# Optimization experiments

Measured on AMD Instinct MI355X. Metric: run time of the kernel, lower is better.

## Reference

```python
import jax, jax.numpy as jnp
import numpy as np

NUM_HEADS = 16
LN_EPS = 1e-5


def setup_inputs() -> dict:
    key = jax.random.key(0)
    ks = jax.random.split(key, 6)
    b, s, d = 2, 2048, 1024
    scale = 1.0 / np.sqrt(d)
    return {
        "x": jax.random.normal(ks[0], (b, s, d), dtype=jnp.float32),
        "W_w": jax.random.normal(ks[1], (3 * d, d), dtype=jnp.float32) * scale,
        "W_b": jax.random.normal(ks[2], (3 * d,), dtype=jnp.float32) * 0.01,
        "proj_w": jax.random.normal(ks[3], (d, d), dtype=jnp.float32) * scale,
        "proj_b": jax.random.normal(ks[4], (d,), dtype=jnp.float32) * 0.01,
        "gamma": jnp.ones((d,), dtype=jnp.float32),
        "beta": jnp.zeros((d,), dtype=jnp.float32),
    }


def reference(x, W_w, W_b, proj_w, proj_b, gamma, beta):
    b, s, d = x.shape
    h = NUM_HEADS
    hd = d // h
    # fused QKV projection: [b,s,3d]
    qkv = x @ W_w.T + W_b
    q, k, v = jnp.split(qkv, 3, axis=-1)
    # [b,s,d] -> [b,h,s,hd]
    q, k, v = (z.reshape(b, s, h, hd).transpose(0, 2, 1, 3) for z in (q, k, v))
    # NOTE: original scales by sqrt(d), not sqrt(head_dim)
    attn = jnp.einsum('bhqd,bhkd->bhqk', q, k) / jnp.sqrt(jnp.asarray(d, x.dtype))
    attn_weights = jax.nn.softmax(attn, axis=-1)  # [b,h,s,s]
    o = jnp.einsum('bhqk,bhkd->bhqd', attn_weights, v)
    o = o.transpose(0, 2, 1, 3).reshape(b, s, d)
    out = o @ proj_w.T + proj_b  # dropout is identity at eval
    y = x + out
    mu = jnp.mean(y, axis=-1, keepdims=True)
    var = jnp.var(y, axis=-1, keepdims=True)
    y_norm = (y - mu) / jnp.sqrt(var + LN_EPS) * gamma + beta
    return (y_norm, attn_weights)
```

## Files before the change

### kernel.cpp

```cpp
#include <hip/hip_runtime.h>
#include <cstdint>

#define BB 2
#define SS 2048
#define DD 1024
#define HH 16
#define HDIM 64
#define MM (BB*SS)
#define N3 (3*DD)

typedef __attribute__((ext_vector_type(4))) float f32x4;
typedef __attribute__((ext_vector_type(8))) __bf16 bf16x8;

static __device__ __forceinline__ unsigned short f2bf_fast(float f) {
  __bf16 h = (__bf16)f;
  return __builtin_bit_cast(unsigned short, h);
}

static __device__ __forceinline__ uint4 pack8f(const float4 a, const float4 b) {
  union { unsigned short us[8]; uint4 v; } pk;
  pk.us[0] = f2bf_fast(a.x); pk.us[1] = f2bf_fast(a.y); pk.us[2] = f2bf_fast(a.z); pk.us[3] = f2bf_fast(a.w);
  pk.us[4] = f2bf_fast(b.x); pk.us[5] = f2bf_fast(b.y); pk.us[6] = f2bf_fast(b.z); pk.us[7] = f2bf_fast(b.w);
  return pk.v;
}

static __device__ __forceinline__ void gload16(const unsigned short* g, unsigned short* l) {
  __builtin_amdgcn_global_load_lds(
      (const __attribute__((address_space(1))) void*)g,
      (__attribute__((address_space(3))) void*)l, 16, 0, 0);
}

__global__ __launch_bounds__(256) void cvt_kernel(
    const float* __restrict__ x, const float* __restrict__ Ww,
    const float* __restrict__ pw,
    unsigned short* __restrict__ xb, unsigned short* __restrict__ Wwb,
    unsigned short* __restrict__ pwb) {
  const size_t i = ((size_t)blockIdx.x * 256 + threadIdx.x) * 8;
  const float* src;
  unsigned short* dst;
  if (i < 4194304u)       { src = x  + i;            dst = xb  + i; }
  else if (i < 7340032u)  { src = Ww + (i - 4194304u); dst = Wwb + (i - 4194304u); }
  else                    { src = pw + (i - 7340032u); dst = pwb + (i - 7340032u); }
  const float4* s4 = (const float4*)src;
  *(uint4*)dst = pack8f(s4[0], s4[1]);
}

__global__ __launch_bounds__(256) void gemm_qkv(
    const unsigned short* __restrict__ xb, const unsigned short* __restrict__ Wwb,
    const float* __restrict__ Wb,
    unsigned short* __restrict__ qb, unsigned short* __restrict__ kb,
    unsigned short* __restrict__ vbT) {
  __shared__ __align__(16) unsigned short As[128 * 32];
  __shared__ __align__(16) unsigned short Bs[128 * 32];
  const int t = threadIdx.x;
  const int l = t & 63, w = t >> 6;
  const int wr = w >> 1, wc = w & 1;
  const int m0 = blockIdx.y * 128, n0 = blockIdx.x * 128;
  f32x4 acc[4][4] = {};

  for (int kt = 0; kt < DD; kt += 32) {
    __syncthreads();
    #pragma unroll
    for (int i = 0; i < 2; ++i) {
      const int row = (i * 4 + w) * 16 + (l >> 2);
      const int cc = (l & 3) * 8;
      gload16(xb  + (size_t)(m0 + row) * DD + kt + cc, &As[(i * 4 + w) * 512]);
      gload16(Wwb + (size_t)(n0 + row) * DD + kt + cc, &Bs[(i * 4 + w) * 512]);
    }
    __syncthreads();
    bf16x8 a[4], b[4];
    #pragma unroll
    for (int i = 0; i < 4; ++i) {
      a[i] = __builtin_bit_cast(bf16x8, *(const uint4*)&As[(wr * 64 + i * 16 + (l & 15)) * 32 + (l >> 4) * 8]);
      b[i] = __builtin_bit_cast(bf16x8, *(const uint4*)&Bs[(wc * 64 + i * 16 + (l & 15)) * 32 + (l >> 4) * 8]);
    }
    #pragma unroll
    for (int i = 0; i < 4; ++i)
      #pragma unroll
      for (int j = 0; j < 4; ++j)
        acc[i][j] = __builtin_amdgcn_mfma_f32_16x16x32_bf16(a[i], b[j], acc[i][j], 0, 0, 0);
  }

  #pragma unroll
  for (int i = 0; i < 4; ++i)
    #pragma unroll
    for (int j = 0; j < 4; ++j)
      #pragma unroll
      for (int r = 0; r < 4; ++r) {
        const int row = m0 + wr * 64 + i * 16 + (l >> 4) * 4 + r;
        const int col = n0 + wc * 64 + j * 16 + (l & 15);
        const float v = acc[i][j][r] + Wb[col];
        const int bidx = row >> 11;
        const int srow = row & 2047;
        const int which = col >> 10;
        const int cc = col & 1023;
        const int head = cc >> 6;
        const int hd = cc & 63;
        if (which == 0) {
          qb[((size_t)((bidx * HH + head) * SS + srow)) * HDIM + hd] = f2bf_fast(v * 0.03125f);
        } else if (which == 1) {
          kb[((size_t)((bidx * HH + head) * SS + srow)) * HDIM + hd] = f2bf_fast(v);
        } else {
          vbT[((size_t)(bidx * HH + head) * HDIM + hd) * SS + srow] = f2bf_fast(v);
        }
      }
}

__global__ __launch_bounds__(256) void attn_kernel(
    const unsigned short* __restrict__ qb,
    const unsigned short* __restrict__ kb,
    const unsigned short* __restrict__ vbT,
    unsigned short* __restrict__ ob,
    float* __restrict__ attn_out) {
  __shared__ __align__(16) unsigned short Ks[2][64 * 72];
  __shared__ __align__(16) unsigned short Vts[2][64 * 72];
  __shared__ __align__(16) unsigned short Ps[4 * 16 * 72];
  const int t = threadIdx.x;
  const int l = t & 63, w = t >> 6;
  const int bh = blockIdx.y;
  const int q0 = blockIdx.x * 64;
  const size_t base = (size_t)bh * SS * HDIM;

  bf16x8 qa[2];
  #pragma unroll
  for (int kc = 0; kc < 2; ++kc)
    qa[kc] = __builtin_bit_cast(bf16x8,
        *(const uint4*)(qb + base + (size_t)(q0 + w * 16 + (l & 15)) * HDIM + kc * 32 + (l >> 4) * 8));

  const int srow = t >> 2;
  const int scol = (t & 3) * 16;
  const unsigned short* kg = kb + base + (size_t)srow * HDIM + scol;
  const unsigned short* vg = vbT + ((size_t)bh * HDIM + srow) * SS + scol;

  float lsum[4] = {0.f, 0.f, 0.f, 0.f};

  {
    const uint4* g = (const uint4*)kg;
    uint4 a0 = g[0], a1 = g[1];
    uint4* d = (uint4*)&Ks[0][srow * 72 + scol];
    d[0] = a0; d[1] = a1;
  }
  __syncthreads();
  for (int kt = 0; kt < SS; kt += 64) {
    const int cur = (kt >> 6) & 1;
    const bool more = (kt + 64) < SS;
    uint4 a0, a1;
    if (more) {
      const uint4* g = (const uint4*)(kg + (size_t)(kt + 64) * HDIM);
      a0 = g[0]; a1 = g[1];
    }
    f32x4 sf[4] = {};
    __builtin_amdgcn_s_setprio(1);
    #pragma unroll
    for (int kc = 0; kc < 2; ++kc)
      #pragma unroll
      for (int n = 0; n < 4; ++n) {
        bf16x8 kf = __builtin_bit_cast(bf16x8, *(const uint4*)&Ks[cur][(n * 16 + (l & 15)) * 72 + kc * 32 + (l >> 4) * 8]);
        sf[n] = __builtin_amdgcn_mfma_f32_16x16x32_bf16(qa[kc], kf, sf[n], 0, 0, 0);
      }
    __builtin_amdgcn_s_setprio(0);
    #pragma unroll
    for (int r = 0; r < 4; ++r)
      lsum[r] += __expf(sf[0][r]) + __expf(sf[1][r]) + __expf(sf[2][r]) + __expf(sf[3][r]);
    if (more) {
      uint4* d = (uint4*)&Ks[cur ^ 1][srow * 72 + scol];
      d[0] = a0; d[1] = a1;
    }
    __syncthreads();
  }

  float rl[4];
  #pragma unroll
  for (int r = 0; r < 4; ++r) {
    float s = lsum[r];
    #pragma unroll
    for (int off = 1; off < 16; off <<= 1) s += __shfl_xor(s, off);
    rl[r] = 1.0f / s;
  }

  f32x4 of[4] = {};
  unsigned short* Pw = &Ps[w * 16 * 72];
  {
    const uint4* g = (const uint4*)kg;
    uint4 a0 = g[0], a1 = g[1];
    const uint4* gv = (const uint4*)vg;
    uint4 b0 = gv[0], b1 = gv[1];
    uint4* d = (uint4*)&Ks[0][srow * 72 + scol];  d[0] = a0; d[1] = a1;
    uint4* dv = (uint4*)&Vts[0][srow * 72 + scol]; dv[0] = b0; dv[1] = b1;
  }
  __syncthreads();
  float* pr0 = attn_out + ((size_t)bh * SS + (q0 + w * 16 + (l >> 4) * 4)) * SS + (l & 15);
  for (int kt = 0; kt < SS; kt += 64) {
    const int cur = (kt >> 6) & 1;
    const bool more = (kt + 64) < SS;
    uint4 a0, a1, b0, b1;
    if (more) {
      const uint4* g = (const uint4*)(kg + (size_t)(kt + 64) * HDIM);
      a0 = g[0]; a1 = g[1];
      const uint4* gv = (const uint4*)(vg + (kt + 64));
      b0 = gv[0]; b1 = gv[1];
    }
    f32x4 sf[4] = {};
    __builtin_amdgcn_s_setprio(1);
    #pragma unroll
    for (int kc = 0; kc < 2; ++kc)
      #pragma unroll
      for (int n = 0; n < 4; ++n) {
        bf16x8 kf = __builtin_bit_cast(bf16x8, *(const uint4*)&Ks[cur][(n * 16 + (l & 15)) * 72 + kc * 32 + (l >> 4) * 8]);
        sf[n] = __builtin_amdgcn_mfma_f32_16x16x32_bf16(qa[kc], kf, sf[n], 0, 0, 0);
      }
    __builtin_amdgcn_s_setprio(0);
    #pragma unroll
    for (int n = 0; n < 4; ++n)
      #pragma unroll
      for (int r = 0; r < 4; ++r) {
        const float p = __expf(sf[n][r]) * rl[r];
        __builtin_nontemporal_store(p, &pr0[(size_t)r * SS + kt + n * 16]);
        Pw[((l >> 4) * 4 + r) * 72 + n * 16 + (l & 15)] = f2bf_fast(p);
      }
    #pragma unroll
    for (int kc = 0; kc < 2; ++kc) {
      bf16x8 pa = __builtin_bit_cast(bf16x8, *(const uint4*)&Pw[(l & 15) * 72 + kc * 32 + (l >> 4) * 8]);
      __builtin_amdgcn_s_setprio(1);
      #pragma unroll
      for (int n = 0; n < 4; ++n) {
        bf16x8 vf = __builtin_bit_cast(bf16x8, *(const uint4*)&Vts[cur][(n * 16 + (l & 15)) * 72 + kc * 32 + (l >> 4) * 8]);
        of[n] = __builtin_amdgcn_mfma_f32_16x16x32_bf16(pa, vf, of[n], 0, 0, 0);
      }
      __builtin_amdgcn_s_setprio(0);
    }
    if (more) {
      uint4* d = (uint4*)&Ks[cur ^ 1][srow * 72 + scol];  d[0] = a0; d[1] = a1;
      uint4* dv = (uint4*)&Vts[cur ^ 1][srow * 72 + scol]; dv[0] = b0; dv[1] = b1;
    }
    __syncthreads();
  }

  const int bidx = bh >> 4, h_ = bh & 15;
  #pragma unroll
  for (int n = 0; n < 4; ++n)
    #pragma unroll
    for (int r = 0; r < 4; ++r) {
      const int lr = (l >> 4) * 4 + r;
      const int srw = q0 + w * 16 + lr;
      const int col = h_ * 64 + n * 16 + (l & 15);
      ob[((size_t)bidx * SS + srw) * DD + col] = f2bf_fast(of[n][r]);
    }
}

__global__ __launch_bounds__(256) void gemm_proj(
    const unsigned short* __restrict__ ob, const unsigned short* __restrict__ pwb,
    const float* __restrict__ pb, const float* __restrict__ x,
    float* __restrict__ y) {
  __shared__ __align__(16) unsigned short As[128 * 32];
  __shared__ __align__(16) unsigned short Bs[128 * 32];
  const int t = threadIdx.x;
  const int l = t & 63, w = t >> 6;
  const int wr = w >> 1, wc = w & 1;
  const int m0 = blockIdx.y * 128, n0 = blockIdx.x * 128;
  f32x4 acc[4][4] = {};

  for (int kt = 0; kt < DD; kt += 32) {
    __syncthreads();
    #pragma unroll
    for (int i = 0; i < 2; ++i) {
      const int row = (i * 4 + w) * 16 + (l >> 2);
      const int cc = (l & 3) * 8;
      gload16(ob  + (size_t)(m0 + row) * DD + kt + cc, &As[(i * 4 + w) * 512]);
      gload16(pwb + (size_t)(n0 + row) * DD + kt + cc, &Bs[(i * 4 + w) * 512]);
    }
    __syncthreads();
    bf16x8 a[4], b[4];
    #pragma unroll
    for (int i = 0; i < 4; ++i) {
      a[i] = __builtin_bit_cast(bf16x8, *(const uint4*)&As[(wr * 64 + i * 16 + (l & 15)) * 32 + (l >> 4) * 8]);
      b[i] = __builtin_bit_cast(bf16x8, *(const uint4*)&Bs[(wc * 64 + i * 16 + (l & 15)) * 32 + (l >> 4) * 8]);
    }
    #pragma unroll
    for (int i = 0; i < 4; ++i)
      #pragma unroll
      for (int j = 0; j < 4; ++j)
        acc[i][j] = __builtin_amdgcn_mfma_f32_16x16x32_bf16(a[i], b[j], acc[i][j], 0, 0, 0);
  }
  #pragma unroll
  for (int i = 0; i < 4; ++i)
    #pragma unroll
    for (int j = 0; j < 4; ++j)
      #pragma unroll
      for (int r = 0; r < 4; ++r) {
        const int row = m0 + wr * 64 + i * 16 + (l >> 4) * 4 + r;
        const int col = n0 + wc * 64 + j * 16 + (l & 15);
        const size_t idx = (size_t)row * DD + col;
        y[idx] = acc[i][j][r] + pb[col] + x[idx];
      }
}

__global__ __launch_bounds__(256) void ln_kernel(
    float* __restrict__ y, const float* __restrict__ gamma,
    const float* __restrict__ beta) {
  const int row = blockIdx.x;
  const int t = threadIdx.x;
  const float4 v = ((const float4*)(y + (size_t)row * DD))[t];
  float s  = v.x + v.y + v.z + v.w;
  float s2 = v.x * v.x + v.y * v.y + v.z * v.z + v.w * v.w;
  #pragma unroll
  for (int off = 1; off < 64; off <<= 1) { s += __shfl_xor(s, off); s2 += __shfl_xor(s2, off); }
  __shared__ float red[8];
  const int l = t & 63, w = t >> 6;
  if (l == 0) { red[w] = s; red[4 + w] = s2; }
  __syncthreads();
  s  = red[0] + red[1] + red[2] + red[3];
  s2 = red[4] + red[5] + red[6] + red[7];
  const float mu = s * (1.0f / DD);
  const float var = s2 * (1.0f / DD) - mu * mu;
  const float rs = rsqrtf(var + 1e-5f);
  const float4 g  = ((const float4*)gamma)[t];
  const float4 be = ((const float4*)beta)[t];
  float4 o;
  o.x = (v.x - mu) * rs * g.x + be.x;
  o.y = (v.y - mu) * rs * g.y + be.y;
  o.z = (v.z - mu) * rs * g.z + be.z;
  o.w = (v.w - mu) * rs * g.w + be.w;
  ((float4*)(y + (size_t)row * DD))[t] = o;
}

extern "C" void kernel_launch(void* const* d_in, const int* in_sizes, int n_in,
                              void* d_out, int out_size, void* d_ws, size_t ws_size,
                              hipStream_t stream) {
  const float* x     = (const float*)d_in[0];
  const float* Ww    = (const float*)d_in[1];
  const float* Wb    = (const float*)d_in[2];
  const float* Pw    = (const float*)d_in[3];
  const float* Pb    = (const float*)d_in[4];
  const float* gamma = (const float*)d_in[5];
  const float* beta  = (const float*)d_in[6];

  float* out      = (float*)d_out;
  float* y_norm   = out;
  float* attn_out = out + (size_t)MM * DD;

  char* ws = (char*)d_ws;
  unsigned short* qb  = (unsigned short*)(ws);
  unsigned short* kb  = (unsigned short*)(ws +  8388608);
  unsigned short* vbT = (unsigned short*)(ws + 16777216);
  unsigned short* ob  = (unsigned short*)(ws + 25165824);
  unsigned short* xb  = (unsigned short*)(ws + 33554432);
  unsigned short* Wwb = (unsigned short*)(ws + 41943040);
  unsigned short* pwb = (unsigned short*)(ws + 48234496);

  cvt_kernel<<<4096, 256, 0, stream>>>(x, Ww, Pw, xb, Wwb, pwb);
  gemm_qkv<<<dim3(N3 / 128, MM / 128), 256, 0, stream>>>(xb, Wwb, Wb, qb, kb, vbT);
  attn_kernel<<<dim3(SS / 64, BB * HH), 256, 0, stream>>>(qb, kb, vbT, ob, attn_out);
  gemm_proj<<<dim3(DD / 128, MM / 128), 256, 0, stream>>>(ob, pwb, Pb, x, y_norm);
  ln_kernel<<<MM, 256, 0, stream>>>(y_norm, gamma, beta);
}
```

Before: 282.1 us.

## Transpose QK MFMA output, vectorize attention-prob stores, use exp2 and swizzle blocks

The QK^T MFMA now has its operands swapped, so each lane holds four consecutive key columns of one query row. Probabilities can then be written as 16-byte nontemporal stores and packed bf16 writes to shared memory, and the row-sum reduction needs only two shuffles. The Q pre-scale gains a log2(e) factor so the hardware exp2 replaces expf. The attention grid is flattened and swizzled so that neighbouring blocks are spread across heads, which changes how K/V reuse is distributed across XCD caches.

```diff
diff --git a/kernel.cpp b/kernel.cpp
--- a/kernel.cpp
+++ b/kernel.cpp
@@ -97,7 +97,7 @@
         const int head = cc >> 6;
         const int hd = cc & 63;
         if (which == 0) {
-          qb[((size_t)((bidx * HH + head) * SS + srow)) * HDIM + hd] = f2bf_fast(v * 0.03125f);
+          qb[((size_t)((bidx * HH + head) * SS + srow)) * HDIM + hd] = f2bf_fast(v * 0.04508422f);
         } else if (which == 1) {
           kb[((size_t)((bidx * HH + head) * SS + srow)) * HDIM + hd] = f2bf_fast(v);
         } else {
@@ -117,8 +117,10 @@
   __shared__ __align__(16) unsigned short Ps[4 * 16 * 72];
   const int t = threadIdx.x;
   const int l = t & 63, w = t >> 6;
-  const int bh = blockIdx.y;
-  const int q0 = blockIdx.x * 64;
+  const int bid = blockIdx.x;
+  const int swz = (bid & 7) * 128 + (bid >> 3);
+  const int bh = swz >> 5;
+  const int q0 = (swz & 31) * 64;
   const size_t base = (size_t)bh * SS * HDIM;
 
   bf16x8 qa[2];
@@ -132,7 +134,7 @@
   const unsigned short* kg = kb + base + (size_t)srow * HDIM + scol;
   const unsigned short* vg = vbT + ((size_t)bh * HDIM + srow) * SS + scol;
 
-  float lsum[4] = {0.f, 0.f, 0.f, 0.f};
+  float lsum = 0.f;
 
   {
     const uint4* g = (const uint4*)kg;
@@ -156,12 +158,14 @@
       #pragma unroll
       for (int n = 0; n < 4; ++n) {
         bf16x8 kf = __builtin_bit_cast(bf16x8, *(const uint4*)&Ks[cur][(n * 16 + (l & 15)) * 72 + kc * 32 + (l >> 4) * 8]);
-        sf[n] = __builtin_amdgcn_mfma_f32_16x16x32_bf16(qa[kc], kf, sf[n], 0, 0, 0);
+        sf[n] = __builtin_amdgcn_mfma_f32_16x16x32_bf16(kf, qa[kc], sf[n], 0, 0, 0);
       }
     __builtin_amdgcn_s_setprio(0);
     #pragma unroll
-    for (int r = 0; r < 4; ++r)
-      lsum[r] += __expf(sf[0][r]) + __expf(sf[1][r]) + __expf(sf[2][r]) + __expf(sf[3][r]);
+    for (int n = 0; n < 4; ++n)
+      #pragma unroll
+      for (int r = 0; r < 4; ++r)
+        lsum += __builtin_amdgcn_exp2f(sf[n][r]);
     if (more) {
       uint4* d = (uint4*)&Ks[cur ^ 1][srow * 72 + scol];
       d[0] = a0; d[1] = a1;
@@ -169,14 +173,9 @@
     __syncthreads();
   }
 
-  float rl[4];
-  #pragma unroll
-  for (int r = 0; r < 4; ++r) {
-    float s = lsum[r];
-    #pragma unroll
-    for (int off = 1; off < 16; off <<= 1) s += __shfl_xor(s, off);
-    rl[r] = 1.0f / s;
-  }
+  lsum += __shfl_xor(lsum, 16);
+  lsum += __shfl_xor(lsum, 32);
+  const float rl = 1.0f / lsum;
 
   f32x4 of[4] = {};
   unsigned short* Pw = &Ps[w * 16 * 72];
@@ -189,7 +188,7 @@
     uint4* dv = (uint4*)&Vts[0][srow * 72 + scol]; dv[0] = b0; dv[1] = b1;
   }
   __syncthreads();
-  float* pr0 = attn_out + ((size_t)bh * SS + (q0 + w * 16 + (l >> 4) * 4)) * SS + (l & 15);
+  float* prow = attn_out + ((size_t)bh * SS + (q0 + w * 16 + (l & 15))) * SS + (l >> 4) * 4;
   for (int kt = 0; kt < SS; kt += 64) {
     const int cur = (kt >> 6) & 1;
     const bool more = (kt + 64) < SS;
@@ -207,17 +206,22 @@
       #pragma unroll
       for (int n = 0; n < 4; ++n) {
         bf16x8 kf = __builtin_bit_cast(bf16x8, *(const uint4*)&Ks[cur][(n * 16 + (l & 15)) * 72 + kc * 32 + (l >> 4) * 8]);
-        sf[n] = __builtin_amdgcn_mfma_f32_16x16x32_bf16(qa[kc], kf, sf[n], 0, 0, 0);
+        sf[n] = __builtin_amdgcn_mfma_f32_16x16x32_bf16(kf, qa[kc], sf[n], 0, 0, 0);
       }
     __builtin_amdgcn_s_setprio(0);
     #pragma unroll
-    for (int n = 0; n < 4; ++n)
-      #pragma unroll
-      for (int r = 0; r < 4; ++r) {
-        const float p = __expf(sf[n][r]) * rl[r];
-        __builtin_nontemporal_store(p, &pr0[(size_t)r * SS + kt + n * 16]);
-        Pw[((l >> 4) * 4 + r) * 72 + n * 16 + (l & 15)] = f2bf_fast(p);
-      }
+    for (int n = 0; n < 4; ++n) {
+      float4 pv;
+      pv.x = __builtin_amdgcn_exp2f(sf[n][0]) * rl;
+      pv.y = __builtin_amdgcn_exp2f(sf[n][1]) * rl;
+      pv.z = __builtin_amdgcn_exp2f(sf[n][2]) * rl;
+      pv.w = __builtin_amdgcn_exp2f(sf[n][3]) * rl;
+      __builtin_nontemporal_store(*(const f32x4*)&pv, (f32x4*)&prow[kt + n * 16]);
+      ushort4 pb4;
+      pb4.x = f2bf_fast(pv.x); pb4.y = f2bf_fast(pv.y);
+      pb4.z = f2bf_fast(pv.z); pb4.w = f2bf_fast(pv.w);
+      *(ushort4*)&Pw[(l & 15) * 72 + n * 16 + (l >> 4) * 4] = pb4;
+    }
     #pragma unroll
     for (int kc = 0; kc < 2; ++kc) {
       bf16x8 pa = __builtin_bit_cast(bf16x8, *(const uint4*)&Pw[(l & 15) * 72 + kc * 32 + (l >> 4) * 8]);
@@ -350,7 +354,7 @@
 
   cvt_kernel<<<4096, 256, 0, stream>>>(x, Ww, Pw, xb, Wwb, pwb);
   gemm_qkv<<<dim3(N3 / 128, MM / 128), 256, 0, stream>>>(xb, Wwb, Wb, qb, kb, vbT);
-  attn_kernel<<<dim3(SS / 64, BB * HH), 256, 0, stream>>>(qb, kb, vbT, ob, attn_out);
+  attn_kernel<<<1024, 256, 0, stream>>>(qb, kb, vbT, ob, attn_out);
   gemm_proj<<<dim3(DD / 128, MM / 128), 256, 0, stream>>>(ob, pwb, Pb, x, y_norm);
   ln_kernel<<<MM, 256, 0, stream>>>(y_norm, gamma, beta);
 }
```

Result: faster. 266.1 us (-5.7%).
